# Kernel optimization log

Hardware: AMD Instinct MI355X
Metric: run time of the kernel (lower is better)

## Reference

```python
import jax, jax.numpy as jnp
import numpy as np

B, L, D, K, NFFT = 4, 8192, 768, 24, 16384


def setup_inputs() -> dict:
    key = jax.random.key(0)
    k1, k2, k3, k4 = jax.random.split(key, 4)
    x = jax.random.normal(k1, (B, L, D), dtype=jnp.float32)
    phi = jax.random.normal(k2, (L, K), dtype=jnp.float32) * 0.1
    M_inputs = jax.random.normal(k3, (D, D), dtype=jnp.float32) * 0.02
    M_filters = jax.random.normal(k4, (K, D), dtype=jnp.float32) * 0.02
    return {"x": x, "phi": phi, "M_inputs": M_inputs, "M_filters": M_filters, "n": NFFT}


def _convolve_approx(u, v, n):
    # u: (B, L, D) projected inputs; v: (L, D) projected filters (per-channel kernels)
    bsz, seq_len, d = u.shape
    sgn = jnp.where(jnp.arange(seq_len) % 2 == 0, 1.0, -1.0).astype(u.dtype)[None, :, None]  # (1,L,1)
    V = jnp.fft.rfft(v.astype(jnp.float32), n=n, axis=0)[None, :, :, None]  # (1,F,D,1)
    U = jnp.stack([u, u * sgn], axis=-1).astype(jnp.float32)  # (B,L,D,2): [plus, sign-flipped]
    Uf = jnp.fft.rfft(U, n=n, axis=1)  # (B,F,D,2)
    conv = jnp.fft.irfft(V * Uf, n=n, axis=1)[:, :seq_len]  # (B,L,D,2)
    U_plus = conv[..., 0]
    U_minus = conv[..., 1] * sgn
    return U_plus, U_minus


def reference(x, phi, M_inputs, M_filters, n):
    x_proj = x @ M_inputs          # (B,L,D)
    phi_proj = phi @ M_filters     # (L,D)
    spectral_plus, spectral_minus = _convolve_approx(x_proj, phi_proj, n)
    return spectral_plus + spectral_minus
```

## Files before the change

### kernel.cpp

```cpp
#include <hip/hip_runtime.h>
#include <stdint.h>

#define B_SZ 4
#define L_SEQ 8192
#define D_CH 768
#define K_F 24
#define NFFT2 8192
#define LDS_BYTES 69632

typedef __attribute__((ext_vector_type(4))) float f32x4;
typedef __attribute__((ext_vector_type(8))) __bf16 bf16x8;

__device__ __forceinline__ uint32_t f2bf1(float f) {
  uint32_t u = __float_as_uint(f);
  return (u + 0x7fffu + ((u >> 16) & 1u)) >> 16;
}
__device__ __forceinline__ uint32_t packbf2(float lo, float hi) {
  return f2bf1(lo) | (f2bf1(hi) << 16);
}
__device__ __forceinline__ float2 unpackbf2(uint32_t v) {
  return float2{__uint_as_float(v << 16), __uint_as_float(v & 0xffff0000u)};
}
__device__ __forceinline__ float2 cmulf(float2 a, float2 b) {
  return float2{a.x * b.x - a.y * b.y, a.x * b.y + a.y * b.x};
}
__device__ __forceinline__ uint32_t pkbf(float lo, float hi) {
  uint32_t r;
  asm("v_cvt_pk_bf16_f32 %0, %1, %2" : "=v"(r) : "v"(lo), "v"(hi));
  return r;
}

__global__ __launch_bounds__(256) void k_mit(const float* __restrict__ Mi,
                                             uint16_t* __restrict__ MiT) {
  int i = blockIdx.x * 256 + threadIdx.x;
  int n = i / 768, e = i - n * 768;
  MiT[i] = (uint16_t)f2bf1(Mi[e * 768 + n]);
}

template <int S>
__device__ __forceinline__ void dft8(float2* x) {
  const float C = 0.70710678118654752f;
  float2 t0{x[0].x + x[4].x, x[0].y + x[4].y}, t1{x[0].x - x[4].x, x[0].y - x[4].y};
  float2 t2{x[2].x + x[6].x, x[2].y + x[6].y}, t3{x[2].x - x[6].x, x[2].y - x[6].y};
  float2 t4{x[1].x + x[5].x, x[1].y + x[5].y}, t5{x[1].x - x[5].x, x[1].y - x[5].y};
  float2 t6{x[3].x + x[7].x, x[3].y + x[7].y}, t7{x[3].x - x[7].x, x[3].y - x[7].y};
  float2 t3r = (S < 0) ? float2{t3.y, -t3.x} : float2{-t3.y, t3.x};
  float2 t7r = (S < 0) ? float2{t7.y, -t7.x} : float2{-t7.y, t7.x};
  float2 e0{t0.x + t2.x, t0.y + t2.y}, e2{t0.x - t2.x, t0.y - t2.y};
  float2 e1{t1.x + t3r.x, t1.y + t3r.y}, e3{t1.x - t3r.x, t1.y - t3r.y};
  float2 o0{t4.x + t6.x, t4.y + t6.y}, o2{t4.x - t6.x, t4.y - t6.y};
  float2 o1{t5.x + t7r.x, t5.y + t7r.y}, o3{t5.x - t7r.x, t5.y - t7r.y};
  float2 o1r = (S < 0) ? float2{C * (o1.x + o1.y), C * (o1.y - o1.x)}
                       : float2{C * (o1.x - o1.y), C * (o1.y + o1.x)};
  float2 o2r = (S < 0) ? float2{o2.y, -o2.x} : float2{-o2.y, o2.x};
  float2 o3r = (S < 0) ? float2{C * (o3.y - o3.x), -C * (o3.x + o3.y)}
                       : float2{-C * (o3.x + o3.y), C * (o3.x - o3.y)};
  x[0] = float2{e0.x + o0.x, e0.y + o0.y};
  x[4] = float2{e0.x - o0.x, e0.y - o0.y};
  x[1] = float2{e1.x + o1r.x, e1.y + o1r.y};
  x[5] = float2{e1.x - o1r.x, e1.y - o1r.y};
  x[2] = float2{e2.x + o2r.x, e2.y + o2r.y};
  x[6] = float2{e2.x - o2r.x, e2.y - o2r.y};
  x[3] = float2{e3.x + o3r.x, e3.y + o3r.y};
  x[7] = float2{e3.x - o3r.x, e3.y - o3r.y};
}

template <int LH, int S, int NT>
__device__ __forceinline__ void pass_r8(float2* a, int tid) {
  constexpr int h = 1 << LH;
  constexpr int st = h + (h >> 4);
  const float ang = (S < 0 ? -6.2831853071795864769f : 6.2831853071795864769f) / (float)(h * 8);
  __syncthreads();
#pragma unroll
  for (int jj = 0; jj < 1024 / NT; ++jj) {
    int j = jj * NT + tid;
    int pos = j & (h - 1);
    int base = ((j >> LH) << (LH + 3)) + pos;
    float2* p = a + (base + (base >> 4));
    float2 x[8];
#pragma unroll
    for (int q = 0; q < 8; ++q) x[q] = p[q * st];
    float sn, cs;
    __sincosf(ang * (float)pos, &sn, &cs);
    float2 w{cs, sn};
    if constexpr (S < 0) {
      dft8<-1>(x);
      float2 wq = w;
      x[1] = cmulf(x[1], wq);
#pragma unroll
      for (int q = 2; q < 8; ++q) {
        wq = cmulf(wq, w);
        x[q] = cmulf(x[q], wq);
      }
    } else {
      float2 wq = w;
      x[1] = cmulf(x[1], wq);
#pragma unroll
      for (int q = 2; q < 8; ++q) {
        wq = cmulf(wq, w);
        x[q] = cmulf(x[q], wq);
      }
      dft8<1>(x);
    }
#pragma unroll
    for (int q = 0; q < 8; ++q) p[q * st] = x[q];
  }
}

__device__ __forceinline__ void p1_fused(float2* a, const uint32_t* __restrict__ row32, int tid) {
#pragma unroll
  for (int jj = 0; jj < 2; ++jj) {
    int j = jj * 512 + tid;
    float2 x[8];
#pragma unroll
    for (int q = 0; q < 4; ++q) x[q] = unpackbf2(row32[j + q * 1024]);
    x[4] = x[5] = x[6] = x[7] = float2{0.f, 0.f};
    dft8<-1>(x);
    float sn, cs;
    __sincosf(-6.2831853071795864769f / 8192.0f * (float)j, &sn, &cs);
    float2 w{cs, sn}, wq = w;
    x[1] = cmulf(x[1], wq);
#pragma unroll
    for (int q = 2; q < 8; ++q) {
      wq = cmulf(wq, w);
      x[q] = cmulf(x[q], wq);
    }
    float2* p = a + (j + (j >> 4));
#pragma unroll
    for (int q = 0; q < 8; ++q) p[q * 1088] = x[q];
  }
}

__device__ __forceinline__ void mid_fused(float2* a, const uint32_t* __restrict__ wrow, int tid) {
  __syncthreads();
#pragma unroll
  for (int jj = 0; jj < 8; ++jj) {
    int j = jj * 512 + tid;
    float2* p = a + (2 * j + ((2 * j) >> 4));
    float2 u = p[0], v = p[1];
    float2 s{u.x + v.x, u.y + v.y}, dd{u.x - v.x, u.y - v.y};
    uint2 wv = *(const uint2*)(wrow + 2 * j);
    s = cmulf(s, unpackbf2(wv.x));
    dd = cmulf(dd, unpackbf2(wv.y));
    p[0] = float2{s.x + dd.x, s.y + dd.y};
    p[1] = float2{s.x - dd.x, s.y - dd.y};
  }
}

__device__ __forceinline__ void last_fused(float2* a, uint32_t* __restrict__ out32, int tid) {
  __syncthreads();
#pragma unroll
  for (int jj = 0; jj < 2; ++jj) {
    int j = jj * 512 + tid;
    float2* p = a + (j + (j >> 4));
    float2 x[8];
#pragma unroll
    for (int q = 0; q < 8; ++q) x[q] = p[q * 1088];
    float sn, cs;
    __sincosf(6.2831853071795864769f / 8192.0f * (float)j, &sn, &cs);
    float2 w{cs, sn}, wq = w;
    x[1] = cmulf(x[1], wq);
#pragma unroll
    for (int q = 2; q < 8; ++q) {
      wq = cmulf(wq, w);
      x[q] = cmulf(x[q], wq);
    }
    dft8<1>(x);
#pragma unroll
    for (int q = 0; q < 4; ++q) out32[j + q * 1024] = packbf2(x[q].x, x[q].y);
  }
}

__global__ __launch_bounds__(256) void k_phi(const float* __restrict__ phi,
                                             float2* __restrict__ Phi2) {
  extern __shared__ float2 buf[];
  int k = blockIdx.x, tid = threadIdx.x;
  const float scale = 2.0f / 8192.0f;
  for (int r = tid; r < 4096; r += 256) {
    buf[r + (r >> 4)] = float2{phi[(2 * r) * K_F + k] * scale, 0.0f};
    int r2i = r + 4096;
    buf[r2i + (r2i >> 4)] = float2{0.0f, 0.0f};
  }
  pass_r8<10, -1, 256>(buf, tid);
  pass_r8<7, -1, 256>(buf, tid);
  pass_r8<4, -1, 256>(buf, tid);
  pass_r8<1, -1, 256>(buf, tid);
  __syncthreads();
  for (int j = tid; j < 4096; j += 256) {
    float2* p = buf + (2 * j + ((2 * j) >> 4));
    float2 u = p[0], v = p[1];
    p[0] = float2{u.x + v.x, u.y + v.y};
    p[1] = float2{u.x - v.x, u.y - v.y};
  }
  __syncthreads();
  for (int f = tid; f < NFFT2; f += 256) Phi2[k * NFFT2 + f] = buf[f + (f >> 4)];
}

__global__ __launch_bounds__(256) void k_w2(const float2* __restrict__ Phi2,
                                            const float* __restrict__ Mf,
                                            uint32_t* __restrict__ W2) {
  __shared__ float2 p[K_F][256];
  __shared__ float mf[K_F][32];
  int tid = threadIdx.x;
  int fc = blockIdx.x & 31, dc = blockIdx.x >> 5;
  int f0 = fc * 256, d0 = dc * 32;
  for (int i = tid; i < K_F * 256; i += 256) {
    int k = i >> 8, fl = i & 255;
    p[k][fl] = Phi2[k * NFFT2 + f0 + fl];
  }
  for (int i = tid; i < K_F * 32; i += 256) {
    int k = i >> 5, dl = i & 31;
    mf[k][dl] = Mf[k * D_CH + d0 + dl];
  }
  __syncthreads();
  for (int dl = 0; dl < 32; ++dl) {
    float re = 0.f, im = 0.f;
#pragma unroll
    for (int k = 0; k < K_F; ++k) {
      float m = mf[k][dl];
      re += m * p[k][tid].x;
      im += m * p[k][tid].y;
    }
    W2[(size_t)(d0 + dl) * NFFT2 + f0 + tid] = packbf2(re, im);
  }
}

__device__ __forceinline__ void gload_lds16(const void* g, void* l) {
  __builtin_amdgcn_global_load_lds(
      (const __attribute__((address_space(1))) void*)g,
      (__attribute__((address_space(3))) void*)l, 16, 0, 0);
}

__global__ __launch_bounds__(256) void k_gemm(const float* __restrict__ X,
                                              const uint16_t* __restrict__ MiT,
                                              uint16_t* __restrict__ Cp) {
  __shared__ uint16_t As[2][128 * 64];
  __shared__ uint16_t Bs[2][128 * 64];
  int tid = threadIdx.x;
  int lane = tid & 63, wid = tid >> 6;
  int p = blockIdx.x;
  int v = (p & 7) * 192 + (p >> 3);
  int bm = v / 6, bn = v % 6;
  int m0 = bm * 128, n0 = bn * 128;
  int wr = wid >> 1, wc = wid & 1;
  int lm = lane & 15, lg = lane >> 4;
  f32x4 acc[4][4] = {};
  float4 fa[8];

#define LOAD_A(k0)                                                       \
  _Pragma("unroll") for (int it = 0; it < 4; ++it) {                     \
    int s = it * 256 + tid;                                              \
    int row = s >> 3, c16 = s & 7;                                       \
    const float* src = X + (size_t)(m0 + row) * 768 + (k0) + c16 * 8;    \
    fa[2 * it] = *(const float4*)src;                                    \
    fa[2 * it + 1] = *(const float4*)(src + 4);                          \
  }
#define STAGE_B(buf, k0)                                                 \
  _Pragma("unroll") for (int it = 0; it < 4; ++it) {                     \
    int s = it * 256 + tid;                                              \
    int row = s >> 3;                                                    \
    int cb = ((s & 7) << 4) ^ ((row & 7) << 4);                          \
    gload_lds16(MiT + (size_t)(n0 + row) * 768 + (k0) + (cb >> 1),       \
                (char*)Bs[buf] + (it * 256 + wid * 64) * 16);            \
  }
#define WRITE_A(buf)                                                     \
  _Pragma("unroll") for (int it = 0; it < 4; ++it) {                     \
    int s = it * 256 + tid;                                              \
    int row = s >> 3, c16 = s & 7;                                       \
    uint4 o;                                                             \
    o.x = pkbf(fa[2 * it].x, fa[2 * it].y);                              \
    o.y = pkbf(fa[2 * it].z, fa[2 * it].w);                              \
    o.z = pkbf(fa[2 * it + 1].x, fa[2 * it + 1].y);                      \
    o.w = pkbf(fa[2 * it + 1].z, fa[2 * it + 1].w);                      \
    *(uint4*)((char*)As[buf] + row * 128 + ((c16 << 4) ^ ((row & 7) << 4))) = o; \
  }

  LOAD_A(0);
  STAGE_B(0, 0);
  WRITE_A(0);
  asm volatile("s_waitcnt vmcnt(0)" ::: "memory");
  __syncthreads();

  int cur = 0;
  for (int kt = 0; kt < 12; ++kt) {
    int k0n = (kt + 1) * 64;
    if (kt < 11) {
      LOAD_A(k0n);
      STAGE_B(cur ^ 1, k0n);
    }
#pragma unroll
    for (int ks = 0; ks < 2; ++ks) {
      int kbyte = (ks * 32 + lg * 8) * 2;
      bf16x8 a[4], b[4];
#pragma unroll
      for (int mi = 0; mi < 4; ++mi) {
        int row = wr * 64 + mi * 16 + lm;
        a[mi] = *(const bf16x8*)((const char*)As[cur] + row * 128 + (kbyte ^ ((row & 7) << 4)));
      }
#pragma unroll
      for (int ni = 0; ni < 4; ++ni) {
        int row = wc * 64 + ni * 16 + lm;
        b[ni] = *(const bf16x8*)((const char*)Bs[cur] + row * 128 + (kbyte ^ ((row & 7) << 4)));
      }
#pragma unroll
      for (int mi = 0; mi < 4; ++mi)
#pragma unroll
        for (int ni = 0; ni < 4; ++ni)
          acc[mi][ni] = __builtin_amdgcn_mfma_f32_16x16x32_bf16(a[mi], b[ni], acc[mi][ni], 0, 0, 0);
    }
    if (kt < 11) WRITE_A(cur ^ 1);
    __syncthreads();
    cur ^= 1;
  }
#undef LOAD_A
#undef STAGE_B
#undef WRITE_A

#pragma unroll
  for (int mi = 0; mi < 4; ++mi) {
#pragma unroll
    for (int ni = 0; ni < 4; ++ni) {
      int mg = m0 + wr * 64 + mi * 16 + lg * 4;
      int dd = n0 + wc * 64 + ni * 16 + lm;
      int bb = mg >> 13, t = mg & 8191;
      f32x4 vv = acc[mi][ni];
      uint2 o;
      o.x = packbf2(vv[0], vv[1]);
      o.y = packbf2(vv[2], vv[3]);
      *(uint2*)(Cp + ((size_t)bb * 768 + dd) * 8192 + t) = o;
    }
  }
}

__global__ __launch_bounds__(512, 4) void k_conv(const uint16_t* __restrict__ xprojT,
                                                 const uint32_t* __restrict__ W2,
                                                 uint16_t* __restrict__ convo) {
  extern __shared__ float2 buf[];
  int tid = threadIdx.x;
  int bd = blockIdx.x;
  int d = bd % 768;
  const uint32_t* row32 = (const uint32_t*)(xprojT + (size_t)bd * 8192);
  p1_fused(buf, row32, tid);
  pass_r8<7, -1, 512>(buf, tid);
  pass_r8<4, -1, 512>(buf, tid);
  pass_r8<1, -1, 512>(buf, tid);
  mid_fused(buf, W2 + (size_t)d * NFFT2, tid);
  pass_r8<1, 1, 512>(buf, tid);
  pass_r8<4, 1, 512>(buf, tid);
  pass_r8<7, 1, 512>(buf, tid);
  last_fused(buf, (uint32_t*)(convo + (size_t)bd * 8192), tid);
}

__global__ __launch_bounds__(256) void k_tr(const uint16_t* __restrict__ convo,
                                            float* __restrict__ out) {
  __shared__ uint16_t tile[64][72];
  int tid = threadIdx.x;
  int bx = blockIdx.x;
  int b = bx / 1536;
  int r = bx - b * 1536;
  int d0 = (r >> 7) << 6;
  int t0 = (r & 127) << 6;
  {
    int rr = tid >> 3;
    int c8 = (tid & 7) << 3;
#pragma unroll
    for (int p = 0; p < 2; ++p) {
      int row = p * 32 + rr;
      uint4 v = *(const uint4*)(convo + ((size_t)(b * 768 + d0 + row)) * 8192 + t0 + c8);
      *(uint4*)&tile[row][c8] = v;
    }
  }
  __syncthreads();
  {
    int c4 = (tid & 15) << 2;
    int tg = tid >> 4;
#pragma unroll
    for (int p = 0; p < 4; ++p) {
      int tt = p * 16 + tg;
      float4 o;
      o.x = __uint_as_float((uint32_t)tile[c4 + 0][tt] << 16);
      o.y = __uint_as_float((uint32_t)tile[c4 + 1][tt] << 16);
      o.z = __uint_as_float((uint32_t)tile[c4 + 2][tt] << 16);
      o.w = __uint_as_float((uint32_t)tile[c4 + 3][tt] << 16);
      *(float4*)(out + ((size_t)b * 8192 + t0 + tt) * 768 + d0 + c4) = o;
    }
  }
}

extern "C" void kernel_launch(void* const* d_in, const int* in_sizes, int n_in,
                              void* d_out, int out_size, void* d_ws, size_t ws_size,
                              hipStream_t stream) {
  const float* x   = (const float*)d_in[0];
  const float* phi = (const float*)d_in[1];
  const float* Mi  = (const float*)d_in[2];
  const float* Mf  = (const float*)d_in[3];
  float* out = (float*)d_out;

  uint16_t* xprojT = (uint16_t*)d_out + 25165824;

  char* ws = (char*)d_ws;
  uint16_t* convo = (uint16_t*)ws;
  uint32_t* W2    = (uint32_t*)(ws + 50331648);
  float2*   Phi2  = (float2*)(ws + 75497472);
  uint16_t* MiT   = (uint16_t*)(ws + 77070336);

  k_mit<<<2304, 256, 0, stream>>>(Mi, MiT);
  k_phi<<<24, 256, LDS_BYTES, stream>>>(phi, Phi2);
  k_w2<<<768, 256, 0, stream>>>(Phi2, Mf, W2);
  k_gemm<<<1536, 256, 0, stream>>>(x, MiT, xprojT);
  k_conv<<<3072, 512, LDS_BYTES, stream>>>(xprojT, W2, convo);
  k_tr<<<6144, 256, 0, stream>>>(convo, out);
}
```

Baseline: 236.5 us.

## Widen GEMM tile to 128x256 with 8 waves and split-phase MFMA scheduling

The input-projection GEMM now uses 512-thread blocks, each computing a 128x256 output tile instead of 128x128. That halves the redundant fp32 loads of X, the A operand, across N-tiles. The K-step is split into two half-phases separated by barriers, with explicit waitcnt, sched_barrier and setprio around the MFMA bursts. It switches to dynamic LDS of 96KB, which limits occupancy per CU. The extra barriers may add sync overhead.

New measurement: 230.1 us. 2.7% less time.

```diff
diff --git a/kernel.cpp b/kernel.cpp
--- a/kernel.cpp
+++ b/kernel.cpp
@@ -7,6 +7,7 @@
 #define K_F 24
 #define NFFT2 8192
 #define LDS_BYTES 69632
+#define GEMM_LDS 98304
 
 typedef __attribute__((ext_vector_type(4))) float f32x4;
 typedef __attribute__((ext_vector_type(8))) __bf16 bf16x8;
@@ -231,90 +232,111 @@
       (__attribute__((address_space(3))) void*)l, 16, 0, 0);
 }
 
-__global__ __launch_bounds__(256) void k_gemm(const float* __restrict__ X,
-                                              const uint16_t* __restrict__ MiT,
-                                              uint16_t* __restrict__ Cp) {
-  __shared__ uint16_t As[2][128 * 64];
-  __shared__ uint16_t Bs[2][128 * 64];
+__global__ __launch_bounds__(512, 2) void k_gemm(const float* __restrict__ X,
+                                                 const uint16_t* __restrict__ MiT,
+                                                 uint16_t* __restrict__ Cp) {
+  extern __shared__ char lds[];
+  char* const As0 = lds;
+  char* const Bs0 = lds + 32768;
   int tid = threadIdx.x;
   int lane = tid & 63, wid = tid >> 6;
   int p = blockIdx.x;
-  int v = (p & 7) * 192 + (p >> 3);
-  int bm = v / 6, bn = v % 6;
-  int m0 = bm * 128, n0 = bn * 128;
-  int wr = wid >> 1, wc = wid & 1;
+  int v = (p & 7) * 96 + (p >> 3);
+  int bm = v / 3, bn = v % 3;
+  int m0 = bm * 128, n0 = bn * 256;
+  int wr = wid >> 2, wc = wid & 3;
   int lm = lane & 15, lg = lane >> 4;
   f32x4 acc[4][4] = {};
-  float4 fa[8];
-
-#define LOAD_A(k0)                                                       \
-  _Pragma("unroll") for (int it = 0; it < 4; ++it) {                     \
-    int s = it * 256 + tid;                                              \
-    int row = s >> 3, c16 = s & 7;                                       \
-    const float* src = X + (size_t)(m0 + row) * 768 + (k0) + c16 * 8;    \
-    fa[2 * it] = *(const float4*)src;                                    \
-    fa[2 * it + 1] = *(const float4*)(src + 4);                          \
-  }
-#define STAGE_B(buf, k0)                                                 \
-  _Pragma("unroll") for (int it = 0; it < 4; ++it) {                     \
-    int s = it * 256 + tid;                                              \
-    int row = s >> 3;                                                    \
-    int cb = ((s & 7) << 4) ^ ((row & 7) << 4);                          \
-    gload_lds16(MiT + (size_t)(n0 + row) * 768 + (k0) + (cb >> 1),       \
-                (char*)Bs[buf] + (it * 256 + wid * 64) * 16);            \
-  }
-#define WRITE_A(buf)                                                     \
-  _Pragma("unroll") for (int it = 0; it < 4; ++it) {                     \
-    int s = it * 256 + tid;                                              \
-    int row = s >> 3, c16 = s & 7;                                       \
-    uint4 o;                                                             \
-    o.x = pkbf(fa[2 * it].x, fa[2 * it].y);                              \
-    o.y = pkbf(fa[2 * it].z, fa[2 * it].w);                              \
-    o.z = pkbf(fa[2 * it + 1].x, fa[2 * it + 1].y);                      \
-    o.w = pkbf(fa[2 * it + 1].z, fa[2 * it + 1].w);                      \
-    *(uint4*)((char*)As[buf] + row * 128 + ((c16 << 4) ^ ((row & 7) << 4))) = o; \
-  }
-
+  float4 fa[4];
+
+#define STAGE_B(bufc, k0)                                              \
+  _Pragma("unroll") for (int it = 0; it < 4; ++it) {                   \
+    int s = it * 512 + tid;                                            \
+    int row = s >> 3;                                                  \
+    int cb = ((s & 7) << 4) ^ ((row & 7) << 4);                        \
+    gload_lds16(MiT + (size_t)(n0 + row) * 768 + (k0) + (cb >> 1),     \
+                Bs0 + (bufc)*32768 + (it * 512 + wid * 64) * 16);      \
+  }
+#define LOAD_A(k0)                                                     \
+  _Pragma("unroll") for (int jt = 0; jt < 2; ++jt) {                   \
+    int s = jt * 512 + tid;                                            \
+    int row = s >> 3, c16 = s & 7;                                     \
+    const float* src = X + (size_t)(m0 + row) * 768 + (k0) + c16 * 8;  \
+    fa[2 * jt] = *(const float4*)src;                                  \
+    fa[2 * jt + 1] = *(const float4*)(src + 4);                        \
+  }
+#define WRITE_A(bufc)                                                  \
+  _Pragma("unroll") for (int jt = 0; jt < 2; ++jt) {                   \
+    int s = jt * 512 + tid;                                            \
+    int row = s >> 3, c16 = s & 7;                                     \
+    uint4 o;                                                           \
+    o.x = pkbf(fa[2 * jt].x, fa[2 * jt].y);                            \
+    o.y = pkbf(fa[2 * jt].z, fa[2 * jt].w);                            \
+    o.z = pkbf(fa[2 * jt + 1].x, fa[2 * jt + 1].y);                    \
+    o.w = pkbf(fa[2 * jt + 1].z, fa[2 * jt + 1].w);                    \
+    *(uint4*)(As0 + (bufc)*16384 + row * 128 + ((c16 << 4) ^ ((row & 7) << 4))) = o; \
+  }
+#define RD_A(dst, bufc, kbyte)                                                         \
+  _Pragma("unroll") for (int i = 0; i < 4; ++i) {                                      \
+    int row = wr * 64 + i * 16 + lm;                                                   \
+    dst[i] = *(const bf16x8*)(As0 + (bufc)*16384 + row * 128 + ((kbyte) ^ ((row & 7) << 4))); \
+  }
+#define RD_B(dst, bufc, kbyte)                                                         \
+  _Pragma("unroll") for (int i = 0; i < 4; ++i) {                                      \
+    int row = wc * 64 + i * 16 + lm;                                                   \
+    dst[i] = *(const bf16x8*)(Bs0 + (bufc)*32768 + row * 128 + ((kbyte) ^ ((row & 7) << 4))); \
+  }
+#define MFMA16(av, bv)                                                        \
+  _Pragma("unroll") for (int mi = 0; mi < 4; ++mi)                            \
+  _Pragma("unroll") for (int ni = 0; ni < 4; ++ni)                            \
+      acc[mi][ni] = __builtin_amdgcn_mfma_f32_16x16x32_bf16(av[mi], bv[ni], acc[mi][ni], 0, 0, 0);
+
+  STAGE_B(0, 0);
   LOAD_A(0);
-  STAGE_B(0, 0);
   WRITE_A(0);
-  asm volatile("s_waitcnt vmcnt(0)" ::: "memory");
-  __syncthreads();
+  asm volatile("s_waitcnt vmcnt(0) lgkmcnt(0)" ::: "memory");
+  __builtin_amdgcn_s_barrier();
 
   int cur = 0;
   for (int kt = 0; kt < 12; ++kt) {
-    int k0n = (kt + 1) * 64;
+    int nxt = cur ^ 1, k0n = (kt + 1) * 64;
+    int kb0 = lg * 16, kb1 = 64 + lg * 16;
     if (kt < 11) {
+      STAGE_B(nxt, k0n);
       LOAD_A(k0n);
-      STAGE_B(cur ^ 1, k0n);
-    }
-#pragma unroll
-    for (int ks = 0; ks < 2; ++ks) {
-      int kbyte = (ks * 32 + lg * 8) * 2;
-      bf16x8 a[4], b[4];
-#pragma unroll
-      for (int mi = 0; mi < 4; ++mi) {
-        int row = wr * 64 + mi * 16 + lm;
-        a[mi] = *(const bf16x8*)((const char*)As[cur] + row * 128 + (kbyte ^ ((row & 7) << 4)));
-      }
-#pragma unroll
-      for (int ni = 0; ni < 4; ++ni) {
-        int row = wc * 64 + ni * 16 + lm;
-        b[ni] = *(const bf16x8*)((const char*)Bs[cur] + row * 128 + (kbyte ^ ((row & 7) << 4)));
-      }
-#pragma unroll
-      for (int mi = 0; mi < 4; ++mi)
-#pragma unroll
-        for (int ni = 0; ni < 4; ++ni)
-          acc[mi][ni] = __builtin_amdgcn_mfma_f32_16x16x32_bf16(a[mi], b[ni], acc[mi][ni], 0, 0, 0);
-    }
-    if (kt < 11) WRITE_A(cur ^ 1);
-    __syncthreads();
-    cur ^= 1;
-  }
+    }
+    {
+      bf16x8 a0[4], b0[4];
+      RD_A(a0, cur, kb0);
+      RD_B(b0, cur, kb0);
+      asm volatile("s_waitcnt lgkmcnt(0)" ::: "memory");
+      __builtin_amdgcn_sched_barrier(0);
+      __builtin_amdgcn_s_setprio(1);
+      MFMA16(a0, b0);
+      __builtin_amdgcn_s_setprio(0);
+    }
+    __builtin_amdgcn_s_barrier();
+    {
+      bf16x8 a1[4], b1[4];
+      RD_A(a1, cur, kb1);
+      RD_B(b1, cur, kb1);
+      asm volatile("s_waitcnt lgkmcnt(0)" ::: "memory");
+      __builtin_amdgcn_sched_barrier(0);
+      __builtin_amdgcn_s_setprio(1);
+      MFMA16(a1, b1);
+      __builtin_amdgcn_s_setprio(0);
+    }
+    if (kt < 11) WRITE_A(nxt);
+    asm volatile("s_waitcnt vmcnt(0) lgkmcnt(0)" ::: "memory");
+    __builtin_amdgcn_s_barrier();
+    cur = nxt;
+  }
+#undef STAGE_B
 #undef LOAD_A
-#undef STAGE_B
 #undef WRITE_A
+#undef RD_A
+#undef RD_B
+#undef MFMA16
 
 #pragma unroll
   for (int mi = 0; mi < 4; ++mi) {
@@ -407,7 +429,7 @@
   k_mit<<<2304, 256, 0, stream>>>(Mi, MiT);
   k_phi<<<24, 256, LDS_BYTES, stream>>>(phi, Phi2);
   k_w2<<<768, 256, 0, stream>>>(Phi2, Mf, W2);
-  k_gemm<<<1536, 256, 0, stream>>>(x, MiT, xprojT);
+  k_gemm<<<768, 512, GEMM_LDS, stream>>>(x, MiT, xprojT);
   k_conv<<<3072, 512, LDS_BYTES, stream>>>(xprojT, W2, convo);
   k_tr<<<6144, 256, 0, stream>>>(convo, out);
 }
```
